# Kernel optimization log

Hardware: AMD Instinct MI355X
Metric: run time of the kernel (lower is better)

The kernel has to match this reference:

```python
import jax, jax.numpy as jnp
import numpy as np

B, H, W = 8, 256, 256
NF = 64          # num_feat
E = 12           # num_expert
D = NF * 4       # token dim = 256
CD = D * E       # expanded dim = 3072


def _lrelu(x):
    return jnp.where(x >= 0, x, 0.2 * x)


def _conv(x, w, stride, pad):
    return jax.lax.conv_general_dilated(
        x, w, (stride, stride), [(pad, pad), (pad, pad)],
        dimension_numbers=('NCHW', 'OIHW', 'NCHW'))


def _bn(x, g, b):
    # training-mode BatchNorm2d: batch statistics over (N, H, W)
    m = jnp.mean(x, axis=(0, 2, 3), keepdims=True)
    v = jnp.var(x, axis=(0, 2, 3), keepdims=True)
    xn = (x - m) * jax.lax.rsqrt(v + 1e-5)
    return xn * g[None, :, None, None] + b[None, :, None, None]


def setup_inputs() -> dict:
    key = jax.random.key(0)
    ks = jax.random.split(key, 16)
    s = 0.05
    d = {}
    d['x'] = jax.random.normal(ks[0], (B, 3, H, W), jnp.float32)
    d['conv0_w'] = jax.random.normal(ks[1], (NF, 3, 3, 3)) * s
    d['conv0_b'] = jnp.zeros((NF,))
    d['conv1_w'] = jax.random.normal(ks[2], (NF, NF, 4, 4)) * s
    d['bn1_g'] = jnp.ones((NF,)); d['bn1_b'] = jnp.zeros((NF,))
    d['conv2_w'] = jax.random.normal(ks[3], (2 * NF, NF, 3, 3)) * s
    d['bn2_g'] = jnp.ones((2 * NF,)); d['bn2_b'] = jnp.zeros((2 * NF,))
    d['conv3_w'] = jax.random.normal(ks[4], (2 * NF, 2 * NF, 4, 4)) * s
    d['bn3_g'] = jnp.ones((2 * NF,)); d['bn3_b'] = jnp.zeros((2 * NF,))
    d['conv4_w'] = jax.random.normal(ks[5], (4 * NF, 2 * NF, 3, 3)) * s
    d['bn4_g'] = jnp.ones((4 * NF,)); d['bn4_b'] = jnp.zeros((4 * NF,))
    d['conv5_w'] = jax.random.normal(ks[6], (4 * NF, 4 * NF, 3, 3)) * s
    d['bn5_g'] = jnp.ones((4 * NF,)); d['bn5_b'] = jnp.zeros((4 * NF,))
    d['conv6_w'] = jax.random.normal(ks[7], (4 * NF, 4 * NF, 3, 3)) * s
    d['bn6_g'] = jnp.ones((4 * NF,)); d['bn6_b'] = jnp.zeros((4 * NF,))
    d['w_gating'] = jax.random.normal(ks[8], (D, E))          # torch.randn init
    d['body_w'] = jax.random.normal(ks[9], (D, CD)) * s       # Linear(c_dim, c_dim*blocks)
    d['body_b'] = jnp.zeros((CD,))
    d['ortho_w'] = jax.random.normal(ks[10], (1, 1, CD))      # OrthorTransform weight
    d['cls_w1'] = jax.random.normal(ks[11], (D, NF // 2)) * s # shared classifier
    d['cls_b1'] = jnp.zeros((NF // 2,))
    d['cls_w2'] = jax.random.normal(ks[12], (NF // 2, 1)) * s
    d['cls_b2'] = jnp.zeros((1,))
    return d


def reference(x, conv0_w, conv0_b, conv1_w, bn1_g, bn1_b, conv2_w, bn2_g, bn2_b,
              conv3_w, bn3_g, bn3_b, conv4_w, bn4_g, bn4_b, conv5_w, bn5_g, bn5_b,
              conv6_w, bn6_g, bn6_b, w_gating, body_w, body_b, ortho_w,
              cls_w1, cls_b1, cls_w2, cls_b2):
    # --- FE conv stack ---
    h = _lrelu(_conv(x, conv0_w, 1, 1) + conv0_b[None, :, None, None])
    h = _lrelu(_bn(_conv(h, conv1_w, 2, 1), bn1_g, bn1_b))
    h = _lrelu(_bn(_conv(h, conv2_w, 1, 1), bn2_g, bn2_b))
    h = _lrelu(_bn(_conv(h, conv3_w, 2, 1), bn3_g, bn3_b))
    h = _lrelu(_bn(_conv(h, conv4_w, 1, 1), bn4_g, bn4_b))
    h = _lrelu(_bn(_conv(h, conv5_w, 1, 1), bn5_g, bn5_b))
    h = _lrelu(_bn(_conv(h, conv6_w, 1, 1), bn6_g, bn6_b))
    b, c, hh, ww = h.shape
    tok = h.reshape(b, c, hh * ww).transpose(0, 2, 1)            # (B, N, D)
    # --- softmax router ---
    routing = jax.nn.softmax(jnp.einsum('bnd,de->bne', tok, w_gating), axis=-1)
    # --- CodeReduction: Linear + lrelu, OrthorTransform multiply, lrelu ---
    feat = _lrelu(tok @ body_w + body_b)                         # (B, N, E*D)
    feat = _lrelu(feat * ortho_w)
    feat = feat.reshape(b, hh * ww, E, D)                        # torch.split chunks
    # --- shared expert MLP on every chunk (all classifiers alias one module) ---
    hid = _lrelu(jnp.einsum('bned,df->bnef', feat, cls_w1) + cls_b1)
    outs = (jnp.einsum('bnef,fo->bneo', hid, cls_w2) + cls_b2)[..., 0]  # (B,N,E)
    # --- top-1 select (equivalent to the torch.where cascade) ---
    idx = jnp.argmax(routing, axis=-1, keepdims=True)
    output = jnp.take_along_axis(outs, idx, axis=-1)             # (B, N, 1)
    return output
```

## Files before the change

### kernel.cpp

```cpp
#include <hip/hip_runtime.h>

__device__ __forceinline__ float lrelu(float x) { return x >= 0.f ? x : 0.2f * x; }

typedef const __attribute__((address_space(1))) void* gas_ptr;
typedef __attribute__((address_space(3))) void* las_ptr;

__global__ __launch_bounds__(256) void conv0_k(const float* __restrict__ x,
                                               const float* __restrict__ w,
                                               const float* __restrict__ bias,
                                               float* __restrict__ out) {
    __shared__ float sIn[3][34][34];
    __shared__ float sW[27][16];
    const int H = 256;
    int tid = threadIdx.x, tx = tid & 31, ty = tid >> 5;
    int tX = (blockIdx.x & 7) * 32, tY = (blockIdx.x >> 3) * 32;
    int b = blockIdx.y, cog = blockIdx.z * 16;
    float acc[4][16] = {};
    const float* inB = x + (size_t)b * 3 * H * H;
    for (int idx = tid; idx < 3 * 1156; idx += 256) {
        int ci = idx / 1156, r = idx % 1156, iy = r / 34, ix = r % 34;
        int gy = tY - 1 + iy, gx = tX - 1 + ix;
        float v = 0.f;
        if ((unsigned)gy < 256u && (unsigned)gx < 256u)
            v = inB[(ci * H + gy) * H + gx];
        sIn[ci][iy][ix] = v;
    }
    for (int idx = tid; idx < 27 * 16; idx += 256) {
        int co = idx & 15, rest = idx >> 4;
        sW[rest][co] = w[(cog + co) * 27 + rest];
    }
    __syncthreads();
#pragma unroll
    for (int ci = 0; ci < 3; ci++)
#pragma unroll
        for (int dy = 0; dy < 3; dy++)
#pragma unroll
            for (int dx = 0; dx < 3; dx++) {
                float a0 = sIn[ci][ty + dy][tx + dx];
                float a1 = sIn[ci][ty + 8 + dy][tx + dx];
                float a2 = sIn[ci][ty + 16 + dy][tx + dx];
                float a3 = sIn[ci][ty + 24 + dy][tx + dx];
                const float* wp = sW[ci * 9 + dy * 3 + dx];
#pragma unroll
                for (int co = 0; co < 16; co++) {
                    float wv = wp[co];
                    acc[0][co] += a0 * wv; acc[1][co] += a1 * wv;
                    acc[2][co] += a2 * wv; acc[3][co] += a3 * wv;
                }
            }
    float* outB = out + (size_t)(b * 64 + cog) * 67080;
#pragma unroll
    for (int co = 0; co < 16; co++) {
        float bv = bias[cog + co];
#pragma unroll
        for (int r = 0; r < 4; r++)
            outB[(size_t)co * 67080 + (size_t)(tY + ty + 8 * r + 1) * 260 +
                 tX + tx + 1] = lrelu(acc[r][co] + bv);
    }
}

template <int COG>
__device__ __forceinline__ void stats_epi(float (&acc)[4][COG], float2* sRed,
                                          double2* part, int cog, int slotBase,
                                          int S, int tid) {
    const int lane = tid & 63, wv = tid >> 6;
    float s[COG], q[COG];
#pragma unroll
    for (int c = 0; c < COG; c++) {
        float ss = 0.f, qq = 0.f;
#pragma unroll
        for (int j = 0; j < 4; j++) { float v = acc[j][c]; ss += v; qq += v * v; }
        s[c] = ss; q[c] = qq;
    }
#pragma unroll
    for (int off = 32; off; off >>= 1)
#pragma unroll
        for (int c = 0; c < COG; c++) {
            s[c] += __shfl_xor(s[c], off);
            q[c] += __shfl_xor(q[c], off);
        }
    if (lane == 0)
#pragma unroll
        for (int c = 0; c < COG; c++) sRed[wv * COG + c] = make_float2(s[c], q[c]);
    __syncthreads();
    if (tid < COG) {
        double ss = 0.0, qq = 0.0;
#pragma unroll
        for (int wvi = 0; wvi < 4; wvi++) {
            float2 p = sRed[wvi * COG + tid];
            ss += (double)p.x; qq += (double)p.y;
        }
        int slot = slotBase + blockIdx.y * gridDim.x + blockIdx.x;
        part[(size_t)(cog + tid) * S + slot] = make_double2(ss, qq);
    }
}

template <int COG>
__global__ __launch_bounds__(256) void c4x4p_k(const float* __restrict__ in,
                                               const float* __restrict__ w,
                                               float* __restrict__ out,
                                               double2* __restrict__ part,
                                               int slotBase, int S,
                                               int Cin, int Cout, int Hin,
                                               int Hp, int Wp,
                                               int oHp, int oWp, int oOff) {
    constexpr int NSF4 = 1122;
    __shared__ float sIn[3][4488];
    __shared__ float sW[3][16 * COG];
    __shared__ float2 sRed[4 * COG];
    __shared__ alignas(16) float sDummy[64];
    const int Hout = Hin >> 1;
    const int tid = threadIdx.x, tx = tid & 31, ty = tid >> 5;
    const bool lane0 = (tid & 63) == 0;
    const int tpr = Hout >> 5;
    const int tX = (blockIdx.x % tpr) * 32, tY = (blockIdx.x / tpr) * 32;
    const int b = blockIdx.y, cog = blockIdx.z * COG;
    const int HWin = Hp * Wp;
    const float* inB = in + (size_t)b * Cin * HWin;
    const int wvbase = tid & ~63;

    int gOff[5]; int lOff[5]; bool act[5]; bool aw[5];
#pragma unroll
    for (int r = 0; r < 5; r++) {
        int idx = tid + r * 256;
        act[r] = idx < NSF4;
        aw[r] = (r * 256 + wvbase) < NSF4;
        int row = idx / 17, c4 = idx % 17;
        gOff[r] = act[r] ? ((2 * tY + row) * Wp + 2 * tX + 4 * c4) : 0;
        lOff[r] = (r * 256 + wvbase) * 4;
    }
    const int wco = tid % COG, wt = tid / COG;
    const int wgo = ((cog + wco) * Cin) * 16 + wt;
    const bool wact = tid < 16 * COG;
    const bool waw = wvbase < 16 * COG;

    float acc[4][COG];
#pragma unroll
    for (int j = 0; j < 4; j++)
#pragma unroll
        for (int c = 0; c < COG; c++) acc[j][c] = 0.f;

    auto STAGE = [&](int t, int buf) {
        const float* p = inB + (size_t)t * HWin;
#pragma unroll
        for (int r = 0; r < 5; r++) {
            float* dst = act[r] ? &sIn[buf][lOff[r]] : sDummy;
            const float* src = act[r] ? (p + gOff[r]) : p;
            if (act[r] || (!aw[r] && lane0))
                __builtin_amdgcn_global_load_lds((gas_ptr)src, (las_ptr)dst,
                                                 16, 0, 0);
        }
        {
            const float* wsrc = wact ? (w + wgo + t * 16) : w;
            float* wdst = wact ? &sW[buf][wvbase] : sDummy;
            if (wact || (!waw && lane0))
                __builtin_amdgcn_global_load_lds((gas_ptr)wsrc, (las_ptr)wdst,
                                                 4, 0, 0);
        }
    };

    const int steps = Cin;
    STAGE(0, 0);
    STAGE(1, 1);
    int cur = 0, nx2 = 2;
    for (int k = 0; k < steps; k++) {
        if (k < steps - 1) asm volatile("s_waitcnt vmcnt(6)" ::: "memory");
        else               asm volatile("s_waitcnt vmcnt(0)" ::: "memory");
        __builtin_amdgcn_sched_barrier(0);
        __builtin_amdgcn_s_barrier();
        __builtin_amdgcn_sched_barrier(0);
        if (k + 2 < steps) STAGE(k + 2, nx2);
        const float* sI = sIn[cur];
        const float* sw = sW[cur];
#pragma unroll
        for (int dy = 0; dy < 4; dy++)
#pragma unroll
            for (int dx = 0; dx < 4; dx++) {
                const float* bp = sI + (2 * ty + dy) * 68 + 2 * tx + dx;
                float a0 = bp[0];
                float a1 = bp[16 * 68];
                float a2 = bp[32 * 68];
                float a3 = bp[48 * 68];
                const float* wp = sw + (dy * 4 + dx) * COG;
#pragma unroll
                for (int c = 0; c < COG; c++) {
                    float wv = wp[c];
                    acc[0][c] += a0 * wv; acc[1][c] += a1 * wv;
                    acc[2][c] += a2 * wv; acc[3][c] += a3 * wv;
                }
            }
        cur = (cur == 2) ? 0 : cur + 1;
        nx2 = (nx2 == 2) ? 0 : nx2 + 1;
    }

    float* outB = out + (size_t)(b * Cout + cog) * oHp * oWp;
#pragma unroll
    for (int c = 0; c < COG; c++)
#pragma unroll
        for (int r = 0; r < 4; r++)
            outB[(size_t)c * oHp * oWp +
                 (size_t)(tY + ty + 8 * r + oOff) * oWp + tX + tx + oOff] =
                acc[r][c];
    stats_epi<COG>(acc, sRed, part, cog, slotBase, S, tid);
}

template <int COG>
__global__ __launch_bounds__(256) void c3x3_k(const float* __restrict__ in,
                                              const float* __restrict__ w,
                                              float* __restrict__ out,
                                              double2* __restrict__ part,
                                              int slotBase, int S,
                                              int Cin, int Cout, int H,
                                              int Hp, int Wp,
                                              int oHp, int oWp, int oOff) {
    constexpr int RS = 36;
    constexpr int CI = 34 * RS;
    constexpr int NSF4 = 612;
    __shared__ float sIn[3][2 * CI];
    __shared__ float sW[3][18 * COG];
    __shared__ float2 sRed[4 * COG];
    __shared__ alignas(16) float sDummy[64];
    const int tid = threadIdx.x, tx = tid & 31, ty = tid >> 5;
    const bool lane0 = (tid & 63) == 0;
    const int tpr = H >> 5;
    const int tX = (blockIdx.x % tpr) * 32, tY = (blockIdx.x / tpr) * 32;
    const int b = blockIdx.y, cog = blockIdx.z * COG;
    const int HWin = Hp * Wp;
    const float* inB = in + (size_t)b * Cin * HWin;
    const int wvbase = tid & ~63;

    int gOff[3]; int lOff[3]; bool act[3]; bool aw[3];
#pragma unroll
    for (int r = 0; r < 3; r++) {
        int idx = tid + r * 256;
        act[r] = idx < NSF4;
        aw[r] = (r * 256 + wvbase) < NSF4;
        int ci = idx / 306, rem = idx % 306;
        int row = rem / 9, c4 = rem % 9;
        gOff[r] = act[r] ? (ci * HWin + (tY + row) * Wp + tX + 4 * c4) : 0;
        lOff[r] = (r * 256 + wvbase) * 4;
    }
    const bool wact = tid < 18 * COG;
    const bool waw = wvbase < 18 * COG;
    int wgo;
    {
        int co = tid % COG, rest = tid / COG;
        int ci = rest / 9, t = rest % 9;
        wgo = ((cog + co) * Cin + ci) * 9 + t;
    }

    float acc[4][COG];
#pragma unroll
    for (int j = 0; j < 4; j++)
#pragma unroll
        for (int c = 0; c < COG; c++) acc[j][c] = 0.f;

    auto STAGE = [&](int t, int buf) {
        const float* p = inB + (size_t)(2 * t) * HWin;
#pragma unroll
        for (int r = 0; r < 3; r++) {
            float* dst = act[r] ? &sIn[buf][lOff[r]] : sDummy;
            const float* src = act[r] ? (p + gOff[r]) : p;
            if (act[r] || (!aw[r] && lane0))
                __builtin_amdgcn_global_load_lds((gas_ptr)src, (las_ptr)dst,
                                                 16, 0, 0);
        }
        {
            const float* wsrc = wact ? (w + (size_t)(2 * t) * 9 + wgo) : w;
            float* wdst = wact ? &sW[buf][wvbase] : sDummy;
            if (wact || (!waw && lane0))
                __builtin_amdgcn_global_load_lds((gas_ptr)wsrc, (las_ptr)wdst,
                                                 4, 0, 0);
        }
    };

    const int steps = Cin >> 1;
    STAGE(0, 0);
    STAGE(1, 1);
    int cur = 0, nx2 = 2;
    for (int k = 0; k < steps; k++) {
        if (k < steps - 1) asm volatile("s_waitcnt vmcnt(4)" ::: "memory");
        else               asm volatile("s_waitcnt vmcnt(0)" ::: "memory");
        __builtin_amdgcn_sched_barrier(0);
        __builtin_amdgcn_s_barrier();
        __builtin_amdgcn_sched_barrier(0);
        if (k + 2 < steps) STAGE(k + 2, nx2);
        const float* sI = sIn[cur];
        const float* sw = sW[cur];
#pragma unroll
        for (int ci = 0; ci < 2; ci++)
#pragma unroll
            for (int dx = 0; dx < 3; dx++) {
                const float* bp = sI + ci * CI + (4 * ty) * RS + tx + dx;
                float a[6];
#pragma unroll
                for (int j = 0; j < 6; j++) a[j] = bp[j * RS];
#pragma unroll
                for (int dy = 0; dy < 3; dy++) {
                    const float* wp = sw + (ci * 9 + dy * 3 + dx) * COG;
#pragma unroll
                    for (int c = 0; c < COG; c++) {
                        float wv = wp[c];
                        acc[0][c] += a[0 + dy] * wv;
                        acc[1][c] += a[1 + dy] * wv;
                        acc[2][c] += a[2 + dy] * wv;
                        acc[3][c] += a[3 + dy] * wv;
                    }
                }
            }
        cur = (cur == 2) ? 0 : cur + 1;
        nx2 = (nx2 == 2) ? 0 : nx2 + 1;
    }

    float* outB = out + (size_t)(b * Cout + cog) * oHp * oWp;
#pragma unroll
    for (int c = 0; c < COG; c++)
#pragma unroll
        for (int j = 0; j < 4; j++)
            outB[(size_t)c * oHp * oWp +
                 (size_t)(tY + 4 * ty + j + oOff) * oWp + tX + tx + oOff] =
                acc[j][c];
    stats_epi<COG>(acc, sRed, part, cog, slotBase, S, tid);
}

__global__ void bnfin_k(const double2* __restrict__ part, int S, int C, double invN,
                        const float* __restrict__ g, const float* __restrict__ bb,
                        float2* __restrict__ ss) {
    int c = threadIdx.x;
    if (c >= C) return;
    double sum = 0.0, sq = 0.0;
    for (int s = 0; s < S; s++) {
        double2 p = part[(size_t)c * S + s];
        sum += p.x; sq += p.y;
    }
    double m = sum * invN;
    double v = sq * invN - m * m;
    double sc = (double)g[c] / sqrt(v + 1e-5);
    ss[c] = make_float2((float)sc, (float)((double)bb[c] - m * sc));
}

__global__ __launch_bounds__(256) void bnact_k(float* __restrict__ p,
                                               const float2* __restrict__ ss,
                                               int C, int H, int W,
                                               int Hp, int Wp) {
    int pc = blockIdx.x;
    int c = pc & (C - 1);
    float2 t = ss ? ss[c] : make_float2(1.f, 0.f);
    bool xf = (ss != nullptr);
    float* pl = p + (size_t)pc * Hp * Wp;
    int n = Hp * Wp;
    for (int i = threadIdx.x; i < n; i += 256) {
        int y = i / Wp, x = i - y * Wp;
        bool inter = (y >= 1) && (y <= H) && (x >= 1) && (x <= W);
        if (!inter) pl[i] = 0.f;
        else if (xf) { float v = pl[i]; pl[i] = lrelu(t.x * v + t.y); }
    }
}

__global__ __launch_bounds__(256) void transp_k(const float* __restrict__ h6,
                                                const float2* __restrict__ ss,
                                                float* __restrict__ tok) {
    __shared__ float sT[32][33];
    int tx = threadIdx.x & 31, ty = threadIdx.x >> 5;
    int n0 = blockIdx.x * 32, d0 = blockIdx.y * 32, b = blockIdx.z;
    const float* hb = h6 + ((size_t)b * 256 + d0) * 4096 + n0;
#pragma unroll
    for (int r = 0; r < 4; r++) {
        int d = ty + 8 * r;
        float2 t = ss[d0 + d];
        sT[d][tx] = lrelu(t.x * hb[d * 4096 + tx] + t.y);
    }
    __syncthreads();
    float* tb = tok + ((size_t)b * 4096 + n0) * 256 + d0;
#pragma unroll
    for (int r = 0; r < 4; r++) {
        int n = ty + 8 * r;
        tb[n * 256 + tx] = sT[tx][n];
    }
}

__global__ __launch_bounds__(256) void token_k(const float* __restrict__ tok,
                                               const float* __restrict__ wg,
                                               const float* __restrict__ bw,
                                               const float* __restrict__ bb,
                                               const float* __restrict__ ow,
                                               const float* __restrict__ w1,
                                               const float* __restrict__ b1,
                                               const float* __restrict__ w2,
                                               const float* __restrict__ b2,
                                               float* __restrict__ outp) {
    __shared__ float sf[4][256];
    const int tid = threadIdx.x, wave = tid >> 6, l = tid & 63;
    const int t = blockIdx.x * 4 + wave;
    const float4 tv = reinterpret_cast<const float4*>(tok + (size_t)t * 256)[l];
    sf[wave][4 * l + 0] = tv.x; sf[wave][4 * l + 1] = tv.y;
    sf[wave][4 * l + 2] = tv.z; sf[wave][4 * l + 3] = tv.w;

    float lg[12];
#pragma unroll
    for (int e = 0; e < 12; e++) lg[e] = 0.f;
    const float tj[4] = {tv.x, tv.y, tv.z, tv.w};
#pragma unroll
    for (int j = 0; j < 4; j++) {
        const float* wr = wg + (4 * l + j) * 12;
#pragma unroll
        for (int e = 0; e < 12; e++) lg[e] += tj[j] * wr[e];
    }
#pragma unroll
    for (int off = 32; off > 0; off >>= 1) {
#pragma unroll
        for (int e = 0; e < 12; e++) lg[e] += __shfl_xor(lg[e], off);
    }
    int idx = 0; float best = lg[0];
#pragma unroll
    for (int e = 1; e < 12; e++)
        if (lg[e] > best) { best = lg[e]; idx = e; }
    const int cb = idx * 256;

    float f0 = 0.f, f1 = 0.f, f2 = 0.f, f3 = 0.f;
    const float* bwp = bw + cb + 4 * l;
#pragma unroll 4
    for (int d = 0; d < 256; d++) {
        const float td = sf[wave][d];
        const float4 wv = *reinterpret_cast<const float4*>(bwp + (size_t)d * 3072);
        f0 += td * wv.x; f1 += td * wv.y;
        f2 += td * wv.z; f3 += td * wv.w;
    }
    float fj[4] = {f0, f1, f2, f3};
#pragma unroll
    for (int j = 0; j < 4; j++) {
        int jj = cb + 4 * l + j;
        float v = lrelu(fj[j] + bb[jj]);
        v = lrelu(v * ow[jj]);
        sf[wave][4 * l + j] = v;
    }

    float o = 0.f;
    if (l < 32) {
        float h = b1[l];
#pragma unroll 4
        for (int j = 0; j < 256; j++) h += sf[wave][j] * w1[j * 32 + l];
        h = lrelu(h);
        o = h * w2[l];
    }
    o += __shfl_xor(o, 16); o += __shfl_xor(o, 8); o += __shfl_xor(o, 4);
    o += __shfl_xor(o, 2);  o += __shfl_xor(o, 1);
    if (l == 0) outp[t] = o + b2[0];
}

extern "C" void kernel_launch(void* const* d_in, const int* in_sizes, int n_in,
                              void* d_out, int out_size, void* d_ws, size_t ws_size,
                              hipStream_t stream) {
    const float* x   = (const float*)d_in[0];
    const float* w0  = (const float*)d_in[1];
    const float* b0  = (const float*)d_in[2];
    const float* w1  = (const float*)d_in[3];
    const float* g1  = (const float*)d_in[4];
    const float* be1 = (const float*)d_in[5];
    const float* w2  = (const float*)d_in[6];
    const float* g2  = (const float*)d_in[7];
    const float* be2 = (const float*)d_in[8];
    const float* w3  = (const float*)d_in[9];
    const float* g3  = (const float*)d_in[10];
    const float* be3 = (const float*)d_in[11];
    const float* w4  = (const float*)d_in[12];
    const float* g4  = (const float*)d_in[13];
    const float* be4 = (const float*)d_in[14];
    const float* w5  = (const float*)d_in[15];
    const float* g5  = (const float*)d_in[16];
    const float* be5 = (const float*)d_in[17];
    const float* w6  = (const float*)d_in[18];
    const float* g6  = (const float*)d_in[19];
    const float* be6 = (const float*)d_in[20];
    const float* wg  = (const float*)d_in[21];
    const float* bw  = (const float*)d_in[22];
    const float* bbp = (const float*)d_in[23];
    const float* owp = (const float*)d_in[24];
    const float* cw1 = (const float*)d_in[25];
    const float* cb1 = (const float*)d_in[26];
    const float* cw2 = (const float*)d_in[27];
    const float* cb2 = (const float*)d_in[28];

    char* W = (char*)d_ws;
    float2* ssb = (float2*)W;
    float2* ss1 = ssb;
    float2* ss2 = ssb + 64;
    float2* ss3 = ssb + 192;
    float2* ss4 = ssb + 320;
    float2* ss5 = ssb + 576;
    float2* ss6 = ssb + 832;
    double2* part = (double2*)(W + 16384);

    char* BIG = W + 278528;
    float* h0p = (float*)(BIG);
    float* h1p = (float*)(BIG + 70287360);
    float* h2p = (float*)(BIG);
    float* h3p = (float*)(BIG + 70287360);
    float* h4p = (float*)(BIG);
    float* h5p = (float*)(BIG + 36765696);
    float* h6  = (float*)(BIG);
    float* tok = (float*)(BIG + 36765696);

    bnact_k<<<256, 256, 0, stream>>>(h0p, nullptr, 64, 256, 256, 258, 260);
    for (int half = 0; half < 2; half++) {
        conv0_k<<<dim3(64, 4, 4), 256, 0, stream>>>(
            x + (size_t)half * 4 * 3 * 65536, w0, b0, h0p);
        c4x4p_k<8><<<dim3(16, 4, 8), 256, 0, stream>>>(
            h0p, w1, h1p + (size_t)half * 4 * 64 * 17160, part, half * 64, 128,
            64, 64, 256, 258, 260, 130, 132, 1);
    }
    bnfin_k<<<1, 256, 0, stream>>>(part, 128, 64, 1.0 / 131072.0, g1, be1, ss1);
    bnact_k<<<512, 256, 0, stream>>>(h1p, ss1, 64, 128, 128, 130, 132);
    c3x3_k<8><<<dim3(16, 8, 16), 256, 0, stream>>>(
        h1p, w2, h2p, part, 0, 128, 64, 128, 128, 130, 132, 130, 132, 1);
    bnfin_k<<<1, 256, 0, stream>>>(part, 128, 128, 1.0 / 131072.0, g2, be2, ss2);
    bnact_k<<<1024, 256, 0, stream>>>(h2p, ss2, 128, 128, 128, 130, 132);
    c4x4p_k<8><<<dim3(4, 8, 16), 256, 0, stream>>>(
        h2p, w3, h3p, part, 0, 32, 128, 128, 128, 130, 132, 66, 68, 1);
    bnfin_k<<<1, 256, 0, stream>>>(part, 32, 128, 1.0 / 32768.0, g3, be3, ss3);
    bnact_k<<<1024, 256, 0, stream>>>(h3p, ss3, 128, 64, 64, 66, 68);
    c3x3_k<8><<<dim3(4, 8, 32), 256, 0, stream>>>(
        h3p, w4, h4p, part, 0, 32, 128, 256, 64, 66, 68, 66, 68, 1);
    bnfin_k<<<1, 256, 0, stream>>>(part, 32, 256, 1.0 / 32768.0, g4, be4, ss4);
    bnact_k<<<2048, 256, 0, stream>>>(h4p, ss4, 256, 64, 64, 66, 68);
    c3x3_k<8><<<dim3(4, 8, 32), 256, 0, stream>>>(
        h4p, w5, h5p, part, 0, 32, 256, 256, 64, 66, 68, 66, 68, 1);
    bnfin_k<<<1, 256, 0, stream>>>(part, 32, 256, 1.0 / 32768.0, g5, be5, ss5);
    bnact_k<<<2048, 256, 0, stream>>>(h5p, ss5, 256, 64, 64, 66, 68);
    c3x3_k<8><<<dim3(4, 8, 32), 256, 0, stream>>>(
        h5p, w6, h6, part, 0, 32, 256, 256, 64, 66, 68, 64, 64, 0);
    bnfin_k<<<1, 256, 0, stream>>>(part, 32, 256, 1.0 / 32768.0, g6, be6, ss6);
    transp_k<<<dim3(128, 8, 8), 256, 0, stream>>>(h6, ss6, tok);
    token_k<<<8192, 256, 0, stream>>>(tok, wg, bw, bbp, owp, cw1, cb1, cw2, cb2,
                                      (float*)d_out);
}
```

Before: 2.668 ms.

## Read conv weights from pre-transposed global buffers and remap threads to row-major 4-wide outputs

Adds a weight-transpose kernel that lays conv weights out as [ci][tap][co] in scratch memory, so the conv kernels read weights straight from global (uniform, cacheable scalar loads) instead of staging them into LDS through global_load_lds. Each thread now computes four horizontally adjacent outputs in one row and loads its input window with float4 LDS reads reused across taps, instead of scalar LDS loads per tap. The waitcnt counts drop by one to match the removed weight load. In exchange, weight reads go through the cache on every step, and the transpose kernels add extra launches. The float4 row reads may also cause LDS bank conflicts.

New measurement: 2.757 ms. +3.3%, slower.

```diff
diff --git a/kernel.cpp b/kernel.cpp
--- a/kernel.cpp
+++ b/kernel.cpp
@@ -59,8 +59,19 @@
     }
 }
 
+__global__ __launch_bounds__(256) void wtr_k(const float* __restrict__ in,
+                                             float* __restrict__ out,
+                                             int Cout, int Cin, int T) {
+    int i = blockIdx.x * 256 + threadIdx.x;
+    int n = Cout * Cin * T;
+    if (i >= n) return;
+    int co = i % Cout; int rest = i / Cout;
+    int t = rest % T;  int ci = rest / T;
+    out[i] = in[(co * Cin + ci) * T + t];
+}
+
 template <int COG>
-__device__ __forceinline__ void stats_epi(float (&acc)[4][COG], float2* sRed,
+__device__ __forceinline__ void stats_epi(float (&acc)[COG][4], float2* sRed,
                                           double2* part, int cog, int slotBase,
                                           int S, int tid) {
     const int lane = tid & 63, wv = tid >> 6;
@@ -69,7 +80,7 @@
     for (int c = 0; c < COG; c++) {
         float ss = 0.f, qq = 0.f;
 #pragma unroll
-        for (int j = 0; j < 4; j++) { float v = acc[j][c]; ss += v; qq += v * v; }
+        for (int j = 0; j < 4; j++) { float v = acc[c][j]; ss += v; qq += v * v; }
         s[c] = ss; q[c] = qq;
     }
 #pragma unroll
@@ -97,7 +108,7 @@
 
 template <int COG>
 __global__ __launch_bounds__(256) void c4x4p_k(const float* __restrict__ in,
-                                               const float* __restrict__ w,
+                                               const float* __restrict__ wT,
                                                float* __restrict__ out,
                                                double2* __restrict__ part,
                                                int slotBase, int S,
@@ -105,12 +116,12 @@
                                                int Hp, int Wp,
                                                int oHp, int oWp, int oOff) {
     constexpr int NSF4 = 1122;
-    __shared__ float sIn[3][4488];
-    __shared__ float sW[3][16 * COG];
+    __shared__ alignas(16) float sIn[3][4488];
     __shared__ float2 sRed[4 * COG];
     __shared__ alignas(16) float sDummy[64];
     const int Hout = Hin >> 1;
-    const int tid = threadIdx.x, tx = tid & 31, ty = tid >> 5;
+    const int tid = threadIdx.x;
+    const int xg = tid & 7, row = tid >> 3;
     const bool lane0 = (tid & 63) == 0;
     const int tpr = Hout >> 5;
     const int tX = (blockIdx.x % tpr) * 32, tY = (blockIdx.x / tpr) * 32;
@@ -125,20 +136,16 @@
         int idx = tid + r * 256;
         act[r] = idx < NSF4;
         aw[r] = (r * 256 + wvbase) < NSF4;
-        int row = idx / 17, c4 = idx % 17;
-        gOff[r] = act[r] ? ((2 * tY + row) * Wp + 2 * tX + 4 * c4) : 0;
+        int rw = idx / 17, c4 = idx % 17;
+        gOff[r] = act[r] ? ((2 * tY + rw) * Wp + 2 * tX + 4 * c4) : 0;
         lOff[r] = (r * 256 + wvbase) * 4;
     }
-    const int wco = tid % COG, wt = tid / COG;
-    const int wgo = ((cog + wco) * Cin) * 16 + wt;
-    const bool wact = tid < 16 * COG;
-    const bool waw = wvbase < 16 * COG;
-
-    float acc[4][COG];
-#pragma unroll
-    for (int j = 0; j < 4; j++)
-#pragma unroll
-        for (int c = 0; c < COG; c++) acc[j][c] = 0.f;
+
+    float acc[COG][4];
+#pragma unroll
+    for (int c = 0; c < COG; c++)
+#pragma unroll
+        for (int j = 0; j < 4; j++) acc[c][j] = 0.f;
 
     auto STAGE = [&](int t, int buf) {
         const float* p = inB + (size_t)t * HWin;
@@ -150,13 +157,6 @@
                 __builtin_amdgcn_global_load_lds((gas_ptr)src, (las_ptr)dst,
                                                  16, 0, 0);
         }
-        {
-            const float* wsrc = wact ? (w + wgo + t * 16) : w;
-            float* wdst = wact ? &sW[buf][wvbase] : sDummy;
-            if (wact || (!waw && lane0))
-                __builtin_amdgcn_global_load_lds((gas_ptr)wsrc, (las_ptr)wdst,
-                                                 4, 0, 0);
-        }
     };
 
     const int steps = Cin;
@@ -164,31 +164,33 @@
     STAGE(1, 1);
     int cur = 0, nx2 = 2;
     for (int k = 0; k < steps; k++) {
-        if (k < steps - 1) asm volatile("s_waitcnt vmcnt(6)" ::: "memory");
+        if (k < steps - 1) asm volatile("s_waitcnt vmcnt(5)" ::: "memory");
         else               asm volatile("s_waitcnt vmcnt(0)" ::: "memory");
         __builtin_amdgcn_sched_barrier(0);
         __builtin_amdgcn_s_barrier();
         __builtin_amdgcn_sched_barrier(0);
         if (k + 2 < steps) STAGE(k + 2, nx2);
-        const float* sI = sIn[cur];
-        const float* sw = sW[cur];
-#pragma unroll
-        for (int dy = 0; dy < 4; dy++)
+        const float* bp = sIn[cur] + (2 * row) * 68 + 8 * xg;
+        const float* wb = wT + (size_t)k * 16 * Cout + cog;
+#pragma unroll
+        for (int dy = 0; dy < 4; dy++) {
+            float4 q0 = *(const float4*)(bp + dy * 68);
+            float4 q1 = *(const float4*)(bp + dy * 68 + 4);
+            float4 q2 = *(const float4*)(bp + dy * 68 + 8);
+            float a[12] = {q0.x, q0.y, q0.z, q0.w, q1.x, q1.y, q1.z, q1.w,
+                           q2.x, q2.y, q2.z, q2.w};
 #pragma unroll
             for (int dx = 0; dx < 4; dx++) {
-                const float* bp = sI + (2 * ty + dy) * 68 + 2 * tx + dx;
-                float a0 = bp[0];
-                float a1 = bp[16 * 68];
-                float a2 = bp[32 * 68];
-                float a3 = bp[48 * 68];
-                const float* wp = sw + (dy * 4 + dx) * COG;
+                const float* wp = wb + (dy * 4 + dx) * Cout;
 #pragma unroll
                 for (int c = 0; c < COG; c++) {
                     float wv = wp[c];
-                    acc[0][c] += a0 * wv; acc[1][c] += a1 * wv;
-                    acc[2][c] += a2 * wv; acc[3][c] += a3 * wv;
+#pragma unroll
+                    for (int j = 0; j < 4; j++)
+                        acc[c][j] += a[2 * j + dx] * wv;
                 }
             }
+        }
         cur = (cur == 2) ? 0 : cur + 1;
         nx2 = (nx2 == 2) ? 0 : nx2 + 1;
     }
@@ -197,16 +199,16 @@
 #pragma unroll
     for (int c = 0; c < COG; c++)
 #pragma unroll
-        for (int r = 0; r < 4; r++)
+        for (int j = 0; j < 4; j++)
             outB[(size_t)c * oHp * oWp +
-                 (size_t)(tY + ty + 8 * r + oOff) * oWp + tX + tx + oOff] =
-                acc[r][c];
+                 (size_t)(tY + row + oOff) * oWp + tX + 4 * xg + j + oOff] =
+                acc[c][j];
     stats_epi<COG>(acc, sRed, part, cog, slotBase, S, tid);
 }
 
 template <int COG>
 __global__ __launch_bounds__(256) void c3x3_k(const float* __restrict__ in,
-                                              const float* __restrict__ w,
+                                              const float* __restrict__ wT,
                                               float* __restrict__ out,
                                               double2* __restrict__ part,
                                               int slotBase, int S,
@@ -216,11 +218,11 @@
     constexpr int RS = 36;
     constexpr int CI = 34 * RS;
     constexpr int NSF4 = 612;
-    __shared__ float sIn[3][2 * CI];
-    __shared__ float sW[3][18 * COG];
+    __shared__ alignas(16) float sIn[3][2 * CI];
     __shared__ float2 sRed[4 * COG];
     __shared__ alignas(16) float sDummy[64];
-    const int tid = threadIdx.x, tx = tid & 31, ty = tid >> 5;
+    const int tid = threadIdx.x;
+    const int xg = tid & 7, row = tid >> 3;
     const bool lane0 = (tid & 63) == 0;
     const int tpr = H >> 5;
     const int tX = (blockIdx.x % tpr) * 32, tY = (blockIdx.x / tpr) * 32;
@@ -236,24 +238,16 @@
         act[r] = idx < NSF4;
         aw[r] = (r * 256 + wvbase) < NSF4;
         int ci = idx / 306, rem = idx % 306;
-        int row = rem / 9, c4 = rem % 9;
-        gOff[r] = act[r] ? (ci * HWin + (tY + row) * Wp + tX + 4 * c4) : 0;
+        int rw = rem / 9, c4 = rem % 9;
+        gOff[r] = act[r] ? (ci * HWin + (tY + rw) * Wp + tX + 4 * c4) : 0;
         lOff[r] = (r * 256 + wvbase) * 4;
     }
-    const bool wact = tid < 18 * COG;
-    const bool waw = wvbase < 18 * COG;
-    int wgo;
-    {
-        int co = tid % COG, rest = tid / COG;
-        int ci = rest / 9, t = rest % 9;
-        wgo = ((cog + co) * Cin + ci) * 9 + t;
-    }
-
-    float acc[4][COG];
-#pragma unroll
-    for (int j = 0; j < 4; j++)
-#pragma unroll
-        for (int c = 0; c < COG; c++) acc[j][c] = 0.f;
+
+    float acc[COG][4];
+#pragma unroll
+    for (int c = 0; c < COG; c++)
+#pragma unroll
+        for (int j = 0; j < 4; j++) acc[c][j] = 0.f;
 
     auto STAGE = [&](int t, int buf) {
         const float* p = inB + (size_t)(2 * t) * HWin;
@@ -265,13 +259,6 @@
                 __builtin_amdgcn_global_load_lds((gas_ptr)src, (las_ptr)dst,
                                                  16, 0, 0);
         }
-        {
-            const float* wsrc = wact ? (w + (size_t)(2 * t) * 9 + wgo) : w;
-            float* wdst = wact ? &sW[buf][wvbase] : sDummy;
-            if (wact || (!waw && lane0))
-                __builtin_amdgcn_global_load_lds((gas_ptr)wsrc, (las_ptr)wdst,
-                                                 4, 0, 0);
-        }
     };
 
     const int steps = Cin >> 1;
@@ -279,35 +266,36 @@
     STAGE(1, 1);
     int cur = 0, nx2 = 2;
     for (int k = 0; k < steps; k++) {
-        if (k < steps - 1) asm volatile("s_waitcnt vmcnt(4)" ::: "memory");
+        if (k < steps - 1) asm volatile("s_waitcnt vmcnt(3)" ::: "memory");
         else               asm volatile("s_waitcnt vmcnt(0)" ::: "memory");
         __builtin_amdgcn_sched_barrier(0);
         __builtin_amdgcn_s_barrier();
         __builtin_amdgcn_sched_barrier(0);
         if (k + 2 < steps) STAGE(k + 2, nx2);
         const float* sI = sIn[cur];
-        const float* sw = sW[cur];
-#pragma unroll
-        for (int ci = 0; ci < 2; ci++)
-#pragma unroll
-            for (int dx = 0; dx < 3; dx++) {
-                const float* bp = sI + ci * CI + (4 * ty) * RS + tx + dx;
-                float a[6];
-#pragma unroll
-                for (int j = 0; j < 6; j++) a[j] = bp[j * RS];
-#pragma unroll
-                for (int dy = 0; dy < 3; dy++) {
-                    const float* wp = sw + (ci * 9 + dy * 3 + dx) * COG;
+#pragma unroll
+        for (int ci = 0; ci < 2; ci++) {
+            const float* bp = sI + ci * CI + row * RS + 4 * xg;
+            const float* wb = wT + ((size_t)(2 * k + ci) * 9) * Cout + cog;
+#pragma unroll
+            for (int dy = 0; dy < 3; dy++) {
+                float4 q0 = *(const float4*)(bp + dy * RS);
+                float4 q1 = *(const float4*)(bp + dy * RS + 4);
+                float a[8] = {q0.x, q0.y, q0.z, q0.w,
+                              q1.x, q1.y, q1.z, q1.w};
+#pragma unroll
+                for (int dx = 0; dx < 3; dx++) {
+                    const float* wp = wb + (dy * 3 + dx) * Cout;
 #pragma unroll
                     for (int c = 0; c < COG; c++) {
                         float wv = wp[c];
-                        acc[0][c] += a[0 + dy] * wv;
-                        acc[1][c] += a[1 + dy] * wv;
-                        acc[2][c] += a[2 + dy] * wv;
-                        acc[3][c] += a[3 + dy] * wv;
+#pragma unroll
+                        for (int j = 0; j < 4; j++)
+                            acc[c][j] += a[j + dx] * wv;
                     }
                 }
             }
+        }
         cur = (cur == 2) ? 0 : cur + 1;
         nx2 = (nx2 == 2) ? 0 : nx2 + 1;
     }
@@ -318,8 +306,8 @@
 #pragma unroll
         for (int j = 0; j < 4; j++)
             outB[(size_t)c * oHp * oWp +
-                 (size_t)(tY + 4 * ty + j + oOff) * oWp + tX + tx + oOff] =
-                acc[j][c];
+                 (size_t)(tY + row + oOff) * oWp + tX + 4 * xg + j + oOff] =
+                acc[c][j];
     stats_epi<COG>(acc, sRed, part, cog, slotBase, S, tid);
 }
 
@@ -500,35 +488,47 @@
     float* h5p = (float*)(BIG + 36765696);
     float* h6  = (float*)(BIG);
     float* tok = (float*)(BIG + 36765696);
-
+    float* wT1 = (float*)(BIG + 105431040);
+    float* wT2 = (float*)(BIG + 105693184);
+    float* wT3 = (float*)(BIG + 105988096);
+    float* wT4 = (float*)(BIG + 88670208);
+    float* wT5 = (float*)(BIG + 89849856);
+    float* wT6 = (float*)(BIG + 92209152);
+
+    wtr_k<<<256, 256, 0, stream>>>(w1, wT1, 64, 64, 16);
+    wtr_k<<<288, 256, 0, stream>>>(w2, wT2, 128, 64, 9);
+    wtr_k<<<1024, 256, 0, stream>>>(w3, wT3, 128, 128, 16);
     bnact_k<<<256, 256, 0, stream>>>(h0p, nullptr, 64, 256, 256, 258, 260);
     for (int half = 0; half < 2; half++) {
         conv0_k<<<dim3(64, 4, 4), 256, 0, stream>>>(
             x + (size_t)half * 4 * 3 * 65536, w0, b0, h0p);
         c4x4p_k<8><<<dim3(16, 4, 8), 256, 0, stream>>>(
-            h0p, w1, h1p + (size_t)half * 4 * 64 * 17160, part, half * 64, 128,
+            h0p, wT1, h1p + (size_t)half * 4 * 64 * 17160, part, half * 64, 128,
             64, 64, 256, 258, 260, 130, 132, 1);
     }
     bnfin_k<<<1, 256, 0, stream>>>(part, 128, 64, 1.0 / 131072.0, g1, be1, ss1);
     bnact_k<<<512, 256, 0, stream>>>(h1p, ss1, 64, 128, 128, 130, 132);
     c3x3_k<8><<<dim3(16, 8, 16), 256, 0, stream>>>(
-        h1p, w2, h2p, part, 0, 128, 64, 128, 128, 130, 132, 130, 132, 1);
+        h1p, wT2, h2p, part, 0, 128, 64, 128, 128, 130, 132, 130, 132, 1);
     bnfin_k<<<1, 256, 0, stream>>>(part, 128, 128, 1.0 / 131072.0, g2, be2, ss2);
     bnact_k<<<1024, 256, 0, stream>>>(h2p, ss2, 128, 128, 128, 130, 132);
     c4x4p_k<8><<<dim3(4, 8, 16), 256, 0, stream>>>(
-        h2p, w3, h3p, part, 0, 32, 128, 128, 128, 130, 132, 66, 68, 1);
+        h2p, wT3, h3p, part, 0, 32, 128, 128, 128, 130, 132, 66, 68, 1);
+    wtr_k<<<1152, 256, 0, stream>>>(w4, wT4, 256, 128, 9);
+    wtr_k<<<2304, 256, 0, stream>>>(w5, wT5, 256, 256, 9);
+    wtr_k<<<2304, 256, 0, stream>>>(w6, wT6, 256, 256, 9);
     bnfin_k<<<1, 256, 0, stream>>>(part, 32, 128, 1.0 / 32768.0, g3, be3, ss3);
     bnact_k<<<1024, 256, 0, stream>>>(h3p, ss3, 128, 64, 64, 66, 68);
     c3x3_k<8><<<dim3(4, 8, 32), 256, 0, stream>>>(
-        h3p, w4, h4p, part, 0, 32, 128, 256, 64, 66, 68, 66, 68, 1);
+        h3p, wT4, h4p, part, 0, 32, 128, 256, 64, 66, 68, 66, 68, 1);
     bnfin_k<<<1, 256, 0, stream>>>(part, 32, 256, 1.0 / 32768.0, g4, be4, ss4);
     bnact_k<<<2048, 256, 0, stream>>>(h4p, ss4, 256, 64, 64, 66, 68);
     c3x3_k<8><<<dim3(4, 8, 32), 256, 0, stream>>>(
-        h4p, w5, h5p, part, 0, 32, 256, 256, 64, 66, 68, 66, 68, 1);
+        h4p, wT5, h5p, part, 0, 32, 256, 256, 64, 66, 68, 66, 68, 1);
     bnfin_k<<<1, 256, 0, stream>>>(part, 32, 256, 1.0 / 32768.0, g5, be5, ss5);
     bnact_k<<<2048, 256, 0, stream>>>(h5p, ss5, 256, 64, 64, 66, 68);
     c3x3_k<8><<<dim3(4, 8, 32), 256, 0, stream>>>(
-        h5p, w6, h6, part, 0, 32, 256, 256, 64, 66, 68, 64, 64, 0);
+        h5p, wT6, h6, part, 0, 32, 256, 256, 64, 66, 68, 64, 64, 0);
     bnfin_k<<<1, 256, 0, stream>>>(part, 32, 256, 1.0 / 32768.0, g6, be6, ss6);
     transp_k<<<dim3(128, 8, 8), 256, 0, stream>>>(h6, ss6, tok);
     token_k<<<8192, 256, 0, stream>>>(tok, wg, bw, bbp, owp, cw1, cb1, cw2, cb2,
```
